# Performance work log

Measured on AMD Instinct MI355X. Metric: run time of the kernel, lower is better.

## Reference

```python
import jax, jax.numpy as jnp
import numpy as np

N, M, D = 1024, 1024, 512


def setup_inputs() -> dict:
    key = jax.random.key(0)
    ks = jax.random.split(key, 12)
    s = 1.0 / np.sqrt(D)
    return {
        "q": jax.random.normal(ks[0], (N, D), jnp.float32),
        "k": jax.random.normal(ks[1], (M, D), jnp.float32),
        "v": jax.random.normal(ks[2], (M, D), jnp.float32),
        "mask": jax.random.randint(ks[3], (N, M), 0, 2) > 0,
        "Wq": jax.random.normal(ks[4], (D, D), jnp.float32) * s,
        "bq": jax.random.normal(ks[5], (D,), jnp.float32) * s,
        "Wk": jax.random.normal(ks[6], (D, D), jnp.float32) * s,
        "bk": jax.random.normal(ks[7], (D,), jnp.float32) * s,
        "Wv": jax.random.normal(ks[8], (D, D), jnp.float32) * s,
        "bv": jax.random.normal(ks[9], (D,), jnp.float32) * s,
        "Ww": jax.random.normal(ks[10], (D,), jnp.float32) * s,
        "bw": jax.random.normal(ks[11], (1,), jnp.float32) * s,
    }


def reference(q, k, v, mask, Wq, bq, Wk, bk, Wv, bv, Ww, bw):
    # Linear projections (torch Linear: x @ W.T + b)
    qp = q @ Wq.T + bq  # [N, D]
    kp = k @ Wk.T + bk  # [M, D]
    vp = v @ Wv.T + bv  # [M, D]
    # Bahdanau additive score: W(tanh(q_n + k_m)) -> [N, M]
    h = jnp.tanh(qp[:, None, :] + kp[None, :, :])  # [N, M, D]
    scores = jnp.einsum('nmd,d->nm', h, Ww) + bw[0]
    scores = jnp.where(mask, scores, jnp.float32(-1000000.0))
    attn = jax.nn.softmax(scores, axis=1)  # softmax over M (dim 1)
    context = jnp.einsum('nm,md->nd', attn, vp)  # [N, D]
    return context
```

## Files before the change

### kernel.cpp

```cpp
#include <hip/hip_runtime.h>
#include <hip/hip_bf16.h>
#include <float.h>


#define NROWS 1024
#define DDIM  512
#define MDIM  1024

typedef __attribute__((ext_vector_type(8))) short s8v;
typedef __attribute__((ext_vector_type(4))) float f4v;
typedef __attribute__((ext_vector_type(2))) float v2f;

__device__ __forceinline__ float bf2f(ushort h) {
    return __uint_as_float(((unsigned)h) << 16);
}
__device__ __forceinline__ ushort2 f2bf2(float a, float b) {
    __hip_bfloat162 t = __float22bfloat162_rn(float2{a, b});
    union { __hip_bfloat162 v; ushort2 u; } c; c.v = t;
    return c.u;
}
__device__ __forceinline__ void hl2(float a, float b, ushort2& h, ushort2& l) {
    h = f2bf2(a, b);
    l = f2bf2(a - bf2f(h.x), b - bf2f(h.y));
}

__global__ __launch_bounds__(256) void proj_gemm(
    const float* __restrict__ q, const float* __restrict__ kk_,
    const float* __restrict__ v,
    const float* __restrict__ Wq, const float* __restrict__ bq,
    const float* __restrict__ Wk, const float* __restrict__ bk,
    const float* __restrict__ Wv, const float* __restrict__ bv,
    float* __restrict__ eq, float* __restrict__ ekT,
    ushort* __restrict__ vph, ushort* __restrict__ vpl,
    float* __restrict__ S, float CS)
{
    __shared__ ushort Ah[4096], Al[4096], Bh[4096], Bl[4096];

    const float* A; const float* B; const float* bias;
    int biasRow;
    if (blockIdx.z == 0)      { A = q;   B = Wq;  bias = bq; biasRow = 0; }
    else if (blockIdx.z == 1) { A = Wk;  B = kk_; bias = bk; biasRow = 1; }
    else                      { A = Wv;  B = v;   bias = bv; biasRow = 1; }

    const int bi = (blockIdx.z == 0) ? blockIdx.x : blockIdx.y;
    const int bj = (blockIdx.z == 0) ? blockIdx.y : blockIdx.x;

    const int t    = threadIdx.x;
    const int lane = t & 63;
    const int w    = t >> 6;
    const int lm   = lane & 15;
    const int lq   = lane >> 4;
    const int i0   = bi * 64;
    const int j0   = bj * 64;
    const int mh   = (w >> 1) * 32;
    const int nh   = (w & 1) * 32;

    if (blockIdx.z == 0) {
        const int jb = blockIdx.x * 8 + blockIdx.y;
        float4 zz = {0.f, 0.f, 0.f, 0.f};
#pragma unroll
        for (int p = 0; p < 8; ++p)
            *(float4*)&S[(size_t)jb * 8192 + (t + p * 256) * 4] = zz;
    }

    f4v acc[2][2] = {{{0.f,0.f,0.f,0.f},{0.f,0.f,0.f,0.f}},
                     {{0.f,0.f,0.f,0.f},{0.f,0.f,0.f,0.f}}};
    float4 pa[4], pb[4];

    const int sr = t >> 4, sc4 = t & 15;
#pragma unroll
    for (int p = 0; p < 4; ++p) {
        int r = sr + p * 16;
        pa[p] = *(const float4*)&A[(size_t)(i0 + r) * DDIM + sc4 * 4];
        pb[p] = *(const float4*)&B[(size_t)(j0 + r) * DDIM + sc4 * 4];
    }

    for (int kc = 0; kc < 8; ++kc) {
        __syncthreads();
#pragma unroll
        for (int p = 0; p < 4; ++p) {
            int r = sr + p * 16;
            int ad = r * 64 + (((sc4 >> 1) ^ (r & 7)) << 3) + (sc4 & 1) * 4;
            ushort2 h01, l01, h23, l23;
            hl2(pa[p].x, pa[p].y, h01, l01);
            hl2(pa[p].z, pa[p].w, h23, l23);
            ushort4 ha = {h01.x, h01.y, h23.x, h23.y};
            ushort4 la = {l01.x, l01.y, l23.x, l23.y};
            *(ushort4*)&Ah[ad] = ha;
            *(ushort4*)&Al[ad] = la;
            hl2(pb[p].x, pb[p].y, h01, l01);
            hl2(pb[p].z, pb[p].w, h23, l23);
            ushort4 hb = {h01.x, h01.y, h23.x, h23.y};
            ushort4 lb = {l01.x, l01.y, l23.x, l23.y};
            *(ushort4*)&Bh[ad] = hb;
            *(ushort4*)&Bl[ad] = lb;
        }
        __syncthreads();
        if (kc < 7) {
            const int k0 = (kc + 1) * 64;
#pragma unroll
            for (int p = 0; p < 4; ++p) {
                int r = sr + p * 16;
                pa[p] = *(const float4*)&A[(size_t)(i0 + r) * DDIM + k0 + sc4 * 4];
                pb[p] = *(const float4*)&B[(size_t)(j0 + r) * DDIM + k0 + sc4 * 4];
            }
        }
#pragma unroll
        for (int ks = 0; ks < 2; ++ks) {
            const int kb = ks * 4 + lq;
            s8v afh[2], afl[2], bfh[2], bfl[2];
#pragma unroll
            for (int g = 0; g < 2; ++g) {
                int ra = mh + g * 16 + lm;
                int rb = nh + g * 16 + lm;
                int aa = ra * 64 + ((kb ^ (ra & 7)) << 3);
                int ab = rb * 64 + ((kb ^ (rb & 7)) << 3);
                afh[g] = *(const s8v*)&Ah[aa];
                afl[g] = *(const s8v*)&Al[aa];
                bfh[g] = *(const s8v*)&Bh[ab];
                bfl[g] = *(const s8v*)&Bl[ab];
            }
#pragma unroll
            for (int mi = 0; mi < 2; ++mi)
#pragma unroll
                for (int ni = 0; ni < 2; ++ni) {
                    acc[mi][ni] = __builtin_amdgcn_mfma_f32_16x16x32_bf16(
                        afh[mi], bfh[ni], acc[mi][ni], 0, 0, 0);
                    acc[mi][ni] = __builtin_amdgcn_mfma_f32_16x16x32_bf16(
                        afh[mi], bfl[ni], acc[mi][ni], 0, 0, 0);
                    acc[mi][ni] = __builtin_amdgcn_mfma_f32_16x16x32_bf16(
                        afl[mi], bfh[ni], acc[mi][ni], 0, 0, 0);
                }
        }
    }

    const float CLAMP = 8192.0f;
#pragma unroll
    for (int mi = 0; mi < 2; ++mi) {
#pragma unroll
        for (int ni = 0; ni < 2; ++ni) {
#pragma unroll
            for (int p = 0; p < 4; ++p) {
                int row = i0 + mh + mi * 16 + lq * 4 + p;
                int col = j0 + nh + ni * 16 + lm;
                float val = acc[mi][ni][p] + (biasRow ? bias[row] : bias[col]);
                if (blockIdx.z == 0) {
                    eq[(size_t)row * 512 + col] =
                        fminf(__builtin_amdgcn_exp2f(val * CS), CLAMP);
                } else if (blockIdx.z == 1) {
                    ekT[(size_t)row * 1024 + col] =
                        fminf(__builtin_amdgcn_exp2f(val * CS), CLAMP);
                } else {
                    ushort2 h2 = f2bf2(val, val);
                    vph[(size_t)row * 1024 + col] = h2.x;
                    ushort2 l2 = f2bf2(val - bf2f(h2.x), 0.f);
                    vpl[(size_t)row * 1024 + col] = l2.x;
                }
            }
        }
    }
}

#define DCH  16
#define SMCH 128
__global__ __launch_bounds__(256) void score_kernel(const float* __restrict__ eq,
                                                    const float* __restrict__ ekT,
                                                    const float* __restrict__ Ww,
                                                    float* __restrict__ S)
{
    __shared__ __align__(16) float ks[DCH * SMCH];
    __shared__ __align__(16) float es[16 * 128];
    __shared__ __align__(16) float wws[128];
    const int t    = threadIdx.x;
    const int lane = t & 63;
    const int w    = t >> 6;
    const int m0   = blockIdx.x * SMCH;
    const int n0   = blockIdx.y * 16;
    const int dbase = blockIdx.z * 128;

    const float SC = 1.220703125e-4f;

#pragma unroll
    for (int p = 0; p < 2; ++p) {
        int idx = t + p * 256;
        int nl = idx >> 5, dd4 = idx & 31;
        float4 e4 = *(const float4*)&eq[(size_t)(n0 + nl) * DDIM + dbase + dd4 * 4];
        float4 e4s = {e4.x * SC, e4.y * SC, e4.z * SC, e4.w * SC};
        *(float4*)&es[nl * 128 + dd4 * 4] = e4s;
    }
    if (t < 128) wws[t] = Ww[dbase + t] * SC;

    const int srow = t >> 5;
    const int scol = (t & 31) * 4;
    const float* gbase = ekT + (size_t)(dbase + srow) * MDIM + m0 + scol;

    float4 ra = *(const float4*)(gbase);
    float4 rb = *(const float4*)(gbase + (size_t)8 * MDIM);
    *(float4*)&ks[srow * SMCH + scol] = ra;
    *(float4*)&ks[(8 + srow) * SMCH + scol] = rb;
    __syncthreads();

    v2f acc[4] = {};
    const v2f cc2 = {1.220703125e-4f, 1.220703125e-4f};

    for (int dc = 0; dc < 128; dc += DCH) {
        if (dc + DCH < 128) {
            const float* g = gbase + (size_t)(dc + DCH) * MDIM;
            ra = *(const float4*)(g);
            rb = *(const float4*)(g + (size_t)8 * MDIM);
        }

#pragma unroll
        for (int dq = 0; dq < DCH; dq += 8) {
            v2f k0 = *(const v2f*)&ks[(dq + 0) * SMCH + lane * 2];
            v2f k1 = *(const v2f*)&ks[(dq + 1) * SMCH + lane * 2];
            v2f k2 = *(const v2f*)&ks[(dq + 2) * SMCH + lane * 2];
            v2f k3 = *(const v2f*)&ks[(dq + 3) * SMCH + lane * 2];
            v2f k4 = *(const v2f*)&ks[(dq + 4) * SMCH + lane * 2];
            v2f k5 = *(const v2f*)&ks[(dq + 5) * SMCH + lane * 2];
            v2f k6 = *(const v2f*)&ks[(dq + 6) * SMCH + lane * 2];
            v2f k7 = *(const v2f*)&ks[(dq + 7) * SMCH + lane * 2];
            float4 wgA = *(const float4*)&wws[dc + dq];
            float4 wgB = *(const float4*)&wws[dc + dq + 4];
#pragma unroll
            for (int nn = 0; nn < 4; ++nn) {
                float4 egA = *(const float4*)&es[(w * 4 + nn) * 128 + dc + dq];
                float4 egB = *(const float4*)&es[(w * 4 + nn) * 128 + dc + dq + 4];
                v2f A0 = __builtin_elementwise_fma(k0, (v2f){egA.x, egA.x}, cc2);
                v2f A1 = __builtin_elementwise_fma(k1, (v2f){egA.y, egA.y}, cc2);
                v2f A2 = __builtin_elementwise_fma(k2, (v2f){egA.z, egA.z}, cc2);
                v2f A3 = __builtin_elementwise_fma(k3, (v2f){egA.w, egA.w}, cc2);
                v2f A4 = __builtin_elementwise_fma(k4, (v2f){egB.x, egB.x}, cc2);
                v2f A5 = __builtin_elementwise_fma(k5, (v2f){egB.y, egB.y}, cc2);
                v2f A6 = __builtin_elementwise_fma(k6, (v2f){egB.z, egB.z}, cc2);
                v2f A7 = __builtin_elementwise_fma(k7, (v2f){egB.w, egB.w}, cc2);
                v2f n01 = __builtin_elementwise_fma((v2f){wgA.y, wgA.y}, A0,
                                                    (v2f){wgA.x, wgA.x} * A1);
                v2f d01 = A0 * A1;
                v2f n23 = __builtin_elementwise_fma((v2f){wgA.w, wgA.w}, A2,
                                                    (v2f){wgA.z, wgA.z} * A3);
                v2f d23 = A2 * A3;
                v2f n45 = __builtin_elementwise_fma((v2f){wgB.y, wgB.y}, A4,
                                                    (v2f){wgB.x, wgB.x} * A5);
                v2f d45 = A4 * A5;
                v2f n67 = __builtin_elementwise_fma((v2f){wgB.w, wgB.w}, A6,
                                                    (v2f){wgB.z, wgB.z} * A7);
                v2f d67 = A6 * A7;
                v2f nA = __builtin_elementwise_fma(n01, d23, n23 * d01);
                v2f dA = d01 * d23;
                v2f nB = __builtin_elementwise_fma(n45, d67, n67 * d45);
                v2f dB = d45 * d67;
                v2f num = __builtin_elementwise_fma(nA, dB, nB * dA);
                v2f den = dA * dB;
                v2f r = {__builtin_amdgcn_rcpf(den.x), __builtin_amdgcn_rcpf(den.y)};
                acc[nn] = __builtin_elementwise_fma(num, r, acc[nn]);
            }
        }

        __syncthreads();
        if (dc + DCH < 128) {
            *(float4*)&ks[srow * SMCH + scol] = ra;
            *(float4*)&ks[(8 + srow) * SMCH + scol] = rb;
        }
        __syncthreads();
    }

    const float C2 = -2.8853900817779268f;
    const int m = m0 + lane * 2;
#pragma unroll
    for (int nn = 0; nn < 4; ++nn) {
        int n = n0 + w * 4 + nn;
        atomicAdd(&S[(size_t)n * MDIM + m],     acc[nn].x * C2);
        atomicAdd(&S[(size_t)n * MDIM + m + 1], acc[nn].y * C2);
    }
}

__global__ __launch_bounds__(256) void combine_kernel(const float* __restrict__ S,
                                                      const int* __restrict__ mask,
                                                      ushort* __restrict__ Ph,
                                                      ushort* __restrict__ Pl,
                                                      float* __restrict__ rsum)
{
    __shared__ float red[4];
    const int n = blockIdx.x, t = threadIdx.x;
    const int lane = t & 63, w = t >> 6;

    float4 s  = *(const float4*)&S[(size_t)n * MDIM + t * 4];
    int4   mk = *(const int4*)&mask[(size_t)n * MDIM + t * 4];
    float p0 = mk.x ? __builtin_amdgcn_exp2f(s.x) : 0.f;
    float p1 = mk.y ? __builtin_amdgcn_exp2f(s.y) : 0.f;
    float p2 = mk.z ? __builtin_amdgcn_exp2f(s.z) : 0.f;
    float p3 = mk.w ? __builtin_amdgcn_exp2f(s.w) : 0.f;

    ushort2 h01, l01, h23, l23;
    hl2(p0, p1, h01, l01);
    hl2(p2, p3, h23, l23);
    ushort4 hv = {h01.x, h01.y, h23.x, h23.y};
    ushort4 lv = {l01.x, l01.y, l23.x, l23.y};
    *(ushort4*)&Ph[(size_t)n * MDIM + t * 4] = hv;
    *(ushort4*)&Pl[(size_t)n * MDIM + t * 4] = lv;

    float rs = (p0 + p1) + (p2 + p3);
#pragma unroll
    for (int off = 32; off; off >>= 1) rs += __shfl_xor(rs, off);
    if (lane == 0) red[w] = rs;
    __syncthreads();
    if (t == 0) rsum[n] = (red[0] + red[1]) + (red[2] + red[3]);
}

__global__ __launch_bounds__(256) void ctx_gemm(const ushort* __restrict__ Ph,
                                                const ushort* __restrict__ Pl,
                                                const ushort* __restrict__ vph,
                                                const ushort* __restrict__ vpl,
                                                const float* __restrict__ rsum,
                                                float* __restrict__ out)
{
    __shared__ __align__(16) float red[3 * 64 * 4];
    const int t    = threadIdx.x;
    const int lane = t & 63;
    const int w    = t >> 6;
    const int lm   = lane & 15;
    const int lq   = lane >> 4;
    const int d0   = blockIdx.x * 16;
    const int n0   = blockIdx.y * 16;
    const int mb   = w * 256;

    const ushort* pAh = Ph  + (size_t)(n0 + lm) * MDIM + mb + lq * 8;
    const ushort* pAl = Pl  + (size_t)(n0 + lm) * MDIM + mb + lq * 8;
    const ushort* pBh = vph + (size_t)(d0 + lm) * MDIM + mb + lq * 8;
    const ushort* pBl = vpl + (size_t)(d0 + lm) * MDIM + mb + lq * 8;

    f4v acc = {0.f, 0.f, 0.f, 0.f};
#pragma unroll 4
    for (int m0 = 0; m0 < 256; m0 += 32) {
        s8v ah = *(const s8v*)(pAh + m0);
        s8v al = *(const s8v*)(pAl + m0);
        s8v bh = *(const s8v*)(pBh + m0);
        s8v bl = *(const s8v*)(pBl + m0);
        acc = __builtin_amdgcn_mfma_f32_16x16x32_bf16(ah, bh, acc, 0, 0, 0);
        acc = __builtin_amdgcn_mfma_f32_16x16x32_bf16(ah, bl, acc, 0, 0, 0);
        acc = __builtin_amdgcn_mfma_f32_16x16x32_bf16(al, bh, acc, 0, 0, 0);
    }

    if (w > 0) *(f4v*)&red[((w - 1) * 64 + lane) * 4] = acc;
    __syncthreads();
    if (w == 0) {
#pragma unroll
        for (int i = 0; i < 3; ++i)
            acc += *(const f4v*)&red[(i * 64 + lane) * 4];
#pragma unroll
        for (int p = 0; p < 4; ++p) {
            int nrow = n0 + lq * 4 + p;
            float inv = __builtin_amdgcn_rcpf(rsum[nrow]);
            out[(size_t)nrow * DDIM + d0 + lm] = acc[p] * inv;
        }
    }
}

extern "C" void kernel_launch(void* const* d_in, const int* in_sizes, int n_in,
                              void* d_out, int out_size, void* d_ws, size_t ws_size,
                              hipStream_t stream)
{
    const float* q    = (const float*)d_in[0];
    const float* k    = (const float*)d_in[1];
    const float* v    = (const float*)d_in[2];
    const int*   mask = (const int*)d_in[3];
    const float* Wq   = (const float*)d_in[4];
    const float* bq   = (const float*)d_in[5];
    const float* Wk   = (const float*)d_in[6];
    const float* bk   = (const float*)d_in[7];
    const float* Wv   = (const float*)d_in[8];
    const float* bv   = (const float*)d_in[9];
    const float* Ww   = (const float*)d_in[10];

    float* ws    = (float*)d_ws;
    float* eq    = ws;
    float* ekT   = ws + 524288;
    ushort* vph  = (ushort*)(ws + 1048576);
    ushort* vpl  = (ushort*)(ws + 1310720);
    float* S     = ws + 1572864;
    float* rsum  = ws + 2621440;
    ushort* Ph   = (ushort*)ws;
    ushort* Pl   = (ushort*)(ws + 524288);
    float* out   = (float*)d_out;

    const float CS = 2.8853900817779268f;

    proj_gemm<<<dim3(16, 8, 3), dim3(256), 0, stream>>>(q, k, v, Wq, bq, Wk, bk,
                                                        Wv, bv, eq, ekT,
                                                        vph, vpl, S, CS);
    score_kernel<<<dim3(8, 64, 4), dim3(256), 0, stream>>>(eq, ekT, Ww, S);
    combine_kernel<<<dim3(1024), dim3(256), 0, stream>>>(S, mask, Ph, Pl, rsum);
    ctx_gemm<<<dim3(32, 64), dim3(256), 0, stream>>>(Ph, Pl, vph, vpl, rsum, out);
}
```

Before: 178.0 us.

## Widen score tile to 4 columns per lane with direct global-to-LDS loads

Each lane of the score kernel now computes 4 key columns instead of 2, doubling the m-tile to 256 and halving the grid in x. Reuse of the q-side and weight values held in registers per LDS read goes up. Key tiles are now staged with global_load_lds instead of register prefetch, so the software double-buffering that overlapped the next chunk's load with compute is gone. The q-side scale factor is folded into the projection epilogue. This trades fewer blocks and no load/compute overlap for more arithmetic per LDS access, plus higher register pressure.

After: 203.2 us. +14.2%, slower.

```diff
diff --git a/kernel.cpp b/kernel.cpp
--- a/kernel.cpp
+++ b/kernel.cpp
@@ -22,6 +22,12 @@
 __device__ __forceinline__ void hl2(float a, float b, ushort2& h, ushort2& l) {
     h = f2bf2(a, b);
     l = f2bf2(a - bf2f(h.x), b - bf2f(h.y));
+}
+
+__device__ __forceinline__ void load_lds16(const float* g, float* l) {
+    __builtin_amdgcn_global_load_lds(
+        (const __attribute__((address_space(1))) void*)g,
+        (__attribute__((address_space(3))) void*)l, 16, 0, 0);
 }
 
 __global__ __launch_bounds__(256) void proj_gemm(
@@ -135,6 +141,7 @@
     }
 
     const float CLAMP = 8192.0f;
+    const float SCw   = 1.220703125e-4f;
 #pragma unroll
     for (int mi = 0; mi < 2; ++mi) {
 #pragma unroll
@@ -146,7 +153,7 @@
                 float val = acc[mi][ni][p] + (biasRow ? bias[row] : bias[col]);
                 if (blockIdx.z == 0) {
                     eq[(size_t)row * 512 + col] =
-                        fminf(__builtin_amdgcn_exp2f(val * CS), CLAMP);
+                        fminf(__builtin_amdgcn_exp2f(val * CS), CLAMP) * SCw;
                 } else if (blockIdx.z == 1) {
                     ekT[(size_t)row * 1024 + col] =
                         fminf(__builtin_amdgcn_exp2f(val * CS), CLAMP);
@@ -162,7 +169,7 @@
 }
 
 #define DCH  16
-#define SMCH 128
+#define SMCH 256
 __global__ __launch_bounds__(256) void score_kernel(const float* __restrict__ eq,
                                                     const float* __restrict__ ekT,
                                                     const float* __restrict__ Ww,
@@ -184,94 +191,98 @@
     for (int p = 0; p < 2; ++p) {
         int idx = t + p * 256;
         int nl = idx >> 5, dd4 = idx & 31;
-        float4 e4 = *(const float4*)&eq[(size_t)(n0 + nl) * DDIM + dbase + dd4 * 4];
-        float4 e4s = {e4.x * SC, e4.y * SC, e4.z * SC, e4.w * SC};
-        *(float4*)&es[nl * 128 + dd4 * 4] = e4s;
+        *(float4*)&es[nl * 128 + dd4 * 4] =
+            *(const float4*)&eq[(size_t)(n0 + nl) * DDIM + dbase + dd4 * 4];
     }
     if (t < 128) wws[t] = Ww[dbase + t] * SC;
 
-    const int srow = t >> 5;
-    const int scol = (t & 31) * 4;
-    const float* gbase = ekT + (size_t)(dbase + srow) * MDIM + m0 + scol;
-
-    float4 ra = *(const float4*)(gbase);
-    float4 rb = *(const float4*)(gbase + (size_t)8 * MDIM);
-    *(float4*)&ks[srow * SMCH + scol] = ra;
-    *(float4*)&ks[(8 + srow) * SMCH + scol] = rb;
-    __syncthreads();
-
-    v2f acc[4] = {};
-    const v2f cc2 = {1.220703125e-4f, 1.220703125e-4f};
+    f4v acc[4] = {};
+    const f4v cc4 = {1.220703125e-4f, 1.220703125e-4f,
+                     1.220703125e-4f, 1.220703125e-4f};
 
     for (int dc = 0; dc < 128; dc += DCH) {
-        if (dc + DCH < 128) {
-            const float* g = gbase + (size_t)(dc + DCH) * MDIM;
-            ra = *(const float4*)(g);
-            rb = *(const float4*)(g + (size_t)8 * MDIM);
-        }
+        __syncthreads();
+#pragma unroll
+        for (int i = 0; i < 4; ++i) {
+            int row = w * 4 + i;
+            const float* g = ekT + (size_t)(dbase + dc + row) * MDIM
+                             + m0 + lane * 4;
+            load_lds16(g, &ks[row * SMCH]);
+        }
+        __syncthreads();
 
 #pragma unroll
         for (int dq = 0; dq < DCH; dq += 8) {
-            v2f k0 = *(const v2f*)&ks[(dq + 0) * SMCH + lane * 2];
-            v2f k1 = *(const v2f*)&ks[(dq + 1) * SMCH + lane * 2];
-            v2f k2 = *(const v2f*)&ks[(dq + 2) * SMCH + lane * 2];
-            v2f k3 = *(const v2f*)&ks[(dq + 3) * SMCH + lane * 2];
-            v2f k4 = *(const v2f*)&ks[(dq + 4) * SMCH + lane * 2];
-            v2f k5 = *(const v2f*)&ks[(dq + 5) * SMCH + lane * 2];
-            v2f k6 = *(const v2f*)&ks[(dq + 6) * SMCH + lane * 2];
-            v2f k7 = *(const v2f*)&ks[(dq + 7) * SMCH + lane * 2];
+            f4v k0 = *(const f4v*)&ks[(dq + 0) * SMCH + lane * 4];
+            f4v k1 = *(const f4v*)&ks[(dq + 1) * SMCH + lane * 4];
+            f4v k2 = *(const f4v*)&ks[(dq + 2) * SMCH + lane * 4];
+            f4v k3 = *(const f4v*)&ks[(dq + 3) * SMCH + lane * 4];
+            f4v k4 = *(const f4v*)&ks[(dq + 4) * SMCH + lane * 4];
+            f4v k5 = *(const f4v*)&ks[(dq + 5) * SMCH + lane * 4];
+            f4v k6 = *(const f4v*)&ks[(dq + 6) * SMCH + lane * 4];
+            f4v k7 = *(const f4v*)&ks[(dq + 7) * SMCH + lane * 4];
             float4 wgA = *(const float4*)&wws[dc + dq];
             float4 wgB = *(const float4*)&wws[dc + dq + 4];
 #pragma unroll
             for (int nn = 0; nn < 4; ++nn) {
                 float4 egA = *(const float4*)&es[(w * 4 + nn) * 128 + dc + dq];
                 float4 egB = *(const float4*)&es[(w * 4 + nn) * 128 + dc + dq + 4];
-                v2f A0 = __builtin_elementwise_fma(k0, (v2f){egA.x, egA.x}, cc2);
-                v2f A1 = __builtin_elementwise_fma(k1, (v2f){egA.y, egA.y}, cc2);
-                v2f A2 = __builtin_elementwise_fma(k2, (v2f){egA.z, egA.z}, cc2);
-                v2f A3 = __builtin_elementwise_fma(k3, (v2f){egA.w, egA.w}, cc2);
-                v2f A4 = __builtin_elementwise_fma(k4, (v2f){egB.x, egB.x}, cc2);
-                v2f A5 = __builtin_elementwise_fma(k5, (v2f){egB.y, egB.y}, cc2);
-                v2f A6 = __builtin_elementwise_fma(k6, (v2f){egB.z, egB.z}, cc2);
-                v2f A7 = __builtin_elementwise_fma(k7, (v2f){egB.w, egB.w}, cc2);
-                v2f n01 = __builtin_elementwise_fma((v2f){wgA.y, wgA.y}, A0,
-                                                    (v2f){wgA.x, wgA.x} * A1);
-                v2f d01 = A0 * A1;
-                v2f n23 = __builtin_elementwise_fma((v2f){wgA.w, wgA.w}, A2,
-                                                    (v2f){wgA.z, wgA.z} * A3);
-                v2f d23 = A2 * A3;
-                v2f n45 = __builtin_elementwise_fma((v2f){wgB.y, wgB.y}, A4,
-                                                    (v2f){wgB.x, wgB.x} * A5);
-                v2f d45 = A4 * A5;
-                v2f n67 = __builtin_elementwise_fma((v2f){wgB.w, wgB.w}, A6,
-                                                    (v2f){wgB.z, wgB.z} * A7);
-                v2f d67 = A6 * A7;
-                v2f nA = __builtin_elementwise_fma(n01, d23, n23 * d01);
-                v2f dA = d01 * d23;
-                v2f nB = __builtin_elementwise_fma(n45, d67, n67 * d45);
-                v2f dB = d45 * d67;
-                v2f num = __builtin_elementwise_fma(nA, dB, nB * dA);
-                v2f den = dA * dB;
-                v2f r = {__builtin_amdgcn_rcpf(den.x), __builtin_amdgcn_rcpf(den.y)};
+                f4v A0 = __builtin_elementwise_fma(k0,
+                         (f4v){egA.x, egA.x, egA.x, egA.x}, cc4);
+                f4v A1 = __builtin_elementwise_fma(k1,
+                         (f4v){egA.y, egA.y, egA.y, egA.y}, cc4);
+                f4v A2 = __builtin_elementwise_fma(k2,
+                         (f4v){egA.z, egA.z, egA.z, egA.z}, cc4);
+                f4v A3 = __builtin_elementwise_fma(k3,
+                         (f4v){egA.w, egA.w, egA.w, egA.w}, cc4);
+                f4v A4 = __builtin_elementwise_fma(k4,
+                         (f4v){egB.x, egB.x, egB.x, egB.x}, cc4);
+                f4v A5 = __builtin_elementwise_fma(k5,
+                         (f4v){egB.y, egB.y, egB.y, egB.y}, cc4);
+                f4v A6 = __builtin_elementwise_fma(k6,
+                         (f4v){egB.z, egB.z, egB.z, egB.z}, cc4);
+                f4v A7 = __builtin_elementwise_fma(k7,
+                         (f4v){egB.w, egB.w, egB.w, egB.w}, cc4);
+                f4v n01 = __builtin_elementwise_fma(
+                    (f4v){wgA.y, wgA.y, wgA.y, wgA.y}, A0,
+                    (f4v){wgA.x, wgA.x, wgA.x, wgA.x} * A1);
+                f4v d01 = A0 * A1;
+                f4v n23 = __builtin_elementwise_fma(
+                    (f4v){wgA.w, wgA.w, wgA.w, wgA.w}, A2,
+                    (f4v){wgA.z, wgA.z, wgA.z, wgA.z} * A3);
+                f4v d23 = A2 * A3;
+                f4v n45 = __builtin_elementwise_fma(
+                    (f4v){wgB.y, wgB.y, wgB.y, wgB.y}, A4,
+                    (f4v){wgB.x, wgB.x, wgB.x, wgB.x} * A5);
+                f4v d45 = A4 * A5;
+                f4v n67 = __builtin_elementwise_fma(
+                    (f4v){wgB.w, wgB.w, wgB.w, wgB.w}, A6,
+                    (f4v){wgB.z, wgB.z, wgB.z, wgB.z} * A7);
+                f4v d67 = A6 * A7;
+                f4v nA = __builtin_elementwise_fma(n01, d23, n23 * d01);
+                f4v dA = d01 * d23;
+                f4v nB = __builtin_elementwise_fma(n45, d67, n67 * d45);
+                f4v dB = d45 * d67;
+                f4v num = __builtin_elementwise_fma(nA, dB, nB * dA);
+                f4v den = dA * dB;
+                f4v r = {__builtin_amdgcn_rcpf(den.x),
+                         __builtin_amdgcn_rcpf(den.y),
+                         __builtin_amdgcn_rcpf(den.z),
+                         __builtin_amdgcn_rcpf(den.w)};
                 acc[nn] = __builtin_elementwise_fma(num, r, acc[nn]);
             }
         }
-
-        __syncthreads();
-        if (dc + DCH < 128) {
-            *(float4*)&ks[srow * SMCH + scol] = ra;
-            *(float4*)&ks[(8 + srow) * SMCH + scol] = rb;
-        }
-        __syncthreads();
     }
 
     const float C2 = -2.8853900817779268f;
-    const int m = m0 + lane * 2;
+    const int m = m0 + lane * 4;
 #pragma unroll
     for (int nn = 0; nn < 4; ++nn) {
         int n = n0 + w * 4 + nn;
         atomicAdd(&S[(size_t)n * MDIM + m],     acc[nn].x * C2);
         atomicAdd(&S[(size_t)n * MDIM + m + 1], acc[nn].y * C2);
+        atomicAdd(&S[(size_t)n * MDIM + m + 2], acc[nn].z * C2);
+        atomicAdd(&S[(size_t)n * MDIM + m + 3], acc[nn].w * C2);
     }
 }
 
@@ -389,7 +400,7 @@
     proj_gemm<<<dim3(16, 8, 3), dim3(256), 0, stream>>>(q, k, v, Wq, bq, Wk, bk,
                                                         Wv, bv, eq, ekT,
                                                         vph, vpl, S, CS);
-    score_kernel<<<dim3(8, 64, 4), dim3(256), 0, stream>>>(eq, ekT, Ww, S);
+    score_kernel<<<dim3(4, 64, 4), dim3(256), 0, stream>>>(eq, ekT, Ww, S);
     combine_kernel<<<dim3(1024), dim3(256), 0, stream>>>(S, mask, Ph, Pl, rsum);
     ctx_gemm<<<dim3(32, 64), dim3(256), 0, stream>>>(Ph, Pl, vph, vpl, rsum, out);
 }
```

## Load key exponentials directly into registers in score kernel, dropping LDS staging

Applied to the files above, without the earlier changes.

The score kernel stops staging ekT tiles through shared memory with double syncthreads per chunk. Each lane now reads its own two key columns straight from global memory into registers, software-pipelined across two 8-row halves. The SC scaling of eq moves into the projection kernel's epilogue so the score kernel copies eq unchanged. The trade-off is that each of the four waves re-reads the same ekT values from global/L2 instead of sharing one LDS copy, and register pressure goes up.

Measured after the change: 179.9 us. No clear change (+1.1%).

```diff
diff --git a/kernel.cpp b/kernel.cpp
--- a/kernel.cpp
+++ b/kernel.cpp
@@ -135,6 +135,7 @@
     }
 
     const float CLAMP = 8192.0f;
+    const float SCw   = 1.220703125e-4f;
 #pragma unroll
     for (int mi = 0; mi < 2; ++mi) {
 #pragma unroll
@@ -146,7 +147,7 @@
                 float val = acc[mi][ni][p] + (biasRow ? bias[row] : bias[col]);
                 if (blockIdx.z == 0) {
                     eq[(size_t)row * 512 + col] =
-                        fminf(__builtin_amdgcn_exp2f(val * CS), CLAMP);
+                        fminf(__builtin_amdgcn_exp2f(val * CS), CLAMP) * SCw;
                 } else if (blockIdx.z == 1) {
                     ekT[(size_t)row * 1024 + col] =
                         fminf(__builtin_amdgcn_exp2f(val * CS), CLAMP);
@@ -161,14 +162,53 @@
     }
 }
 
-#define DCH  16
 #define SMCH 128
+
+#define TREE8(K0,K1,K2,K3,K4,K5,K6,K7,DCQ)                                     \
+    {                                                                          \
+        float4 wgA = *(const float4*)&wws[(DCQ)];                              \
+        float4 wgB = *(const float4*)&wws[(DCQ) + 4];                          \
+        _Pragma("unroll")                                                      \
+        for (int nn = 0; nn < 4; ++nn) {                                       \
+            float4 egA = *(const float4*)&es[(wrow + nn) * 128 + (DCQ)];       \
+            float4 egB = *(const float4*)&es[(wrow + nn) * 128 + (DCQ) + 4];   \
+            v2f A0 = __builtin_elementwise_fma(K0, (v2f){egA.x, egA.x}, cc2);  \
+            v2f A1 = __builtin_elementwise_fma(K1, (v2f){egA.y, egA.y}, cc2);  \
+            v2f A2 = __builtin_elementwise_fma(K2, (v2f){egA.z, egA.z}, cc2);  \
+            v2f A3 = __builtin_elementwise_fma(K3, (v2f){egA.w, egA.w}, cc2);  \
+            v2f A4 = __builtin_elementwise_fma(K4, (v2f){egB.x, egB.x}, cc2);  \
+            v2f A5 = __builtin_elementwise_fma(K5, (v2f){egB.y, egB.y}, cc2);  \
+            v2f A6 = __builtin_elementwise_fma(K6, (v2f){egB.z, egB.z}, cc2);  \
+            v2f A7 = __builtin_elementwise_fma(K7, (v2f){egB.w, egB.w}, cc2);  \
+            v2f n01 = __builtin_elementwise_fma((v2f){wgA.y, wgA.y}, A0,       \
+                                                (v2f){wgA.x, wgA.x} * A1);     \
+            v2f d01 = A0 * A1;                                                 \
+            v2f n23 = __builtin_elementwise_fma((v2f){wgA.w, wgA.w}, A2,       \
+                                                (v2f){wgA.z, wgA.z} * A3);     \
+            v2f d23 = A2 * A3;                                                 \
+            v2f n45 = __builtin_elementwise_fma((v2f){wgB.y, wgB.y}, A4,       \
+                                                (v2f){wgB.x, wgB.x} * A5);     \
+            v2f d45 = A4 * A5;                                                 \
+            v2f n67 = __builtin_elementwise_fma((v2f){wgB.w, wgB.w}, A6,       \
+                                                (v2f){wgB.z, wgB.z} * A7);     \
+            v2f d67 = A6 * A7;                                                 \
+            v2f nA = __builtin_elementwise_fma(n01, d23, n23 * d01);           \
+            v2f dA = d01 * d23;                                                \
+            v2f nB = __builtin_elementwise_fma(n45, d67, n67 * d45);           \
+            v2f dB = d45 * d67;                                                \
+            v2f num = __builtin_elementwise_fma(nA, dB, nB * dA);              \
+            v2f den = dA * dB;                                                 \
+            v2f r = {__builtin_amdgcn_rcpf(den.x),                             \
+                     __builtin_amdgcn_rcpf(den.y)};                            \
+            acc[nn] = __builtin_elementwise_fma(num, r, acc[nn]);              \
+        }                                                                      \
+    }
+
 __global__ __launch_bounds__(256) void score_kernel(const float* __restrict__ eq,
                                                     const float* __restrict__ ekT,
                                                     const float* __restrict__ Ww,
                                                     float* __restrict__ S)
 {
-    __shared__ __align__(16) float ks[DCH * SMCH];
     __shared__ __align__(16) float es[16 * 128];
     __shared__ __align__(16) float wws[128];
     const int t    = threadIdx.x;
@@ -177,6 +217,7 @@
     const int m0   = blockIdx.x * SMCH;
     const int n0   = blockIdx.y * 16;
     const int dbase = blockIdx.z * 128;
+    const int wrow = w * 4;
 
     const float SC = 1.220703125e-4f;
 
@@ -184,92 +225,60 @@
     for (int p = 0; p < 2; ++p) {
         int idx = t + p * 256;
         int nl = idx >> 5, dd4 = idx & 31;
-        float4 e4 = *(const float4*)&eq[(size_t)(n0 + nl) * DDIM + dbase + dd4 * 4];
-        float4 e4s = {e4.x * SC, e4.y * SC, e4.z * SC, e4.w * SC};
-        *(float4*)&es[nl * 128 + dd4 * 4] = e4s;
+        *(float4*)&es[nl * 128 + dd4 * 4] =
+            *(const float4*)&eq[(size_t)(n0 + nl) * DDIM + dbase + dd4 * 4];
     }
     if (t < 128) wws[t] = Ww[dbase + t] * SC;
 
-    const int srow = t >> 5;
-    const int scol = (t & 31) * 4;
-    const float* gbase = ekT + (size_t)(dbase + srow) * MDIM + m0 + scol;
-
-    float4 ra = *(const float4*)(gbase);
-    float4 rb = *(const float4*)(gbase + (size_t)8 * MDIM);
-    *(float4*)&ks[srow * SMCH + scol] = ra;
-    *(float4*)&ks[(8 + srow) * SMCH + scol] = rb;
+    const float* gk = ekT + (size_t)dbase * MDIM + m0 + lane * 2;
+
+    v2f a0 = *(const v2f*)(gk + (size_t)0 * MDIM);
+    v2f a1 = *(const v2f*)(gk + (size_t)1 * MDIM);
+    v2f a2 = *(const v2f*)(gk + (size_t)2 * MDIM);
+    v2f a3 = *(const v2f*)(gk + (size_t)3 * MDIM);
+    v2f a4 = *(const v2f*)(gk + (size_t)4 * MDIM);
+    v2f a5 = *(const v2f*)(gk + (size_t)5 * MDIM);
+    v2f a6 = *(const v2f*)(gk + (size_t)6 * MDIM);
+    v2f a7 = *(const v2f*)(gk + (size_t)7 * MDIM);
+
     __syncthreads();
 
     v2f acc[4] = {};
     const v2f cc2 = {1.220703125e-4f, 1.220703125e-4f};
 
-    for (int dc = 0; dc < 128; dc += DCH) {
-        if (dc + DCH < 128) {
-            const float* g = gbase + (size_t)(dc + DCH) * MDIM;
-            ra = *(const float4*)(g);
-            rb = *(const float4*)(g + (size_t)8 * MDIM);
-        }
-
-#pragma unroll
-        for (int dq = 0; dq < DCH; dq += 8) {
-            v2f k0 = *(const v2f*)&ks[(dq + 0) * SMCH + lane * 2];
-            v2f k1 = *(const v2f*)&ks[(dq + 1) * SMCH + lane * 2];
-            v2f k2 = *(const v2f*)&ks[(dq + 2) * SMCH + lane * 2];
-            v2f k3 = *(const v2f*)&ks[(dq + 3) * SMCH + lane * 2];
-            v2f k4 = *(const v2f*)&ks[(dq + 4) * SMCH + lane * 2];
-            v2f k5 = *(const v2f*)&ks[(dq + 5) * SMCH + lane * 2];
-            v2f k6 = *(const v2f*)&ks[(dq + 6) * SMCH + lane * 2];
-            v2f k7 = *(const v2f*)&ks[(dq + 7) * SMCH + lane * 2];
-            float4 wgA = *(const float4*)&wws[dc + dq];
-            float4 wgB = *(const float4*)&wws[dc + dq + 4];
-#pragma unroll
-            for (int nn = 0; nn < 4; ++nn) {
-                float4 egA = *(const float4*)&es[(w * 4 + nn) * 128 + dc + dq];
-                float4 egB = *(const float4*)&es[(w * 4 + nn) * 128 + dc + dq + 4];
-                v2f A0 = __builtin_elementwise_fma(k0, (v2f){egA.x, egA.x}, cc2);
-                v2f A1 = __builtin_elementwise_fma(k1, (v2f){egA.y, egA.y}, cc2);
-                v2f A2 = __builtin_elementwise_fma(k2, (v2f){egA.z, egA.z}, cc2);
-                v2f A3 = __builtin_elementwise_fma(k3, (v2f){egA.w, egA.w}, cc2);
-                v2f A4 = __builtin_elementwise_fma(k4, (v2f){egB.x, egB.x}, cc2);
-                v2f A5 = __builtin_elementwise_fma(k5, (v2f){egB.y, egB.y}, cc2);
-                v2f A6 = __builtin_elementwise_fma(k6, (v2f){egB.z, egB.z}, cc2);
-                v2f A7 = __builtin_elementwise_fma(k7, (v2f){egB.w, egB.w}, cc2);
-                v2f n01 = __builtin_elementwise_fma((v2f){wgA.y, wgA.y}, A0,
-                                                    (v2f){wgA.x, wgA.x} * A1);
-                v2f d01 = A0 * A1;
-                v2f n23 = __builtin_elementwise_fma((v2f){wgA.w, wgA.w}, A2,
-                                                    (v2f){wgA.z, wgA.z} * A3);
-                v2f d23 = A2 * A3;
-                v2f n45 = __builtin_elementwise_fma((v2f){wgB.y, wgB.y}, A4,
-                                                    (v2f){wgB.x, wgB.x} * A5);
-                v2f d45 = A4 * A5;
-                v2f n67 = __builtin_elementwise_fma((v2f){wgB.w, wgB.w}, A6,
-                                                    (v2f){wgB.z, wgB.z} * A7);
-                v2f d67 = A6 * A7;
-                v2f nA = __builtin_elementwise_fma(n01, d23, n23 * d01);
-                v2f dA = d01 * d23;
-                v2f nB = __builtin_elementwise_fma(n45, d67, n67 * d45);
-                v2f dB = d45 * d67;
-                v2f num = __builtin_elementwise_fma(nA, dB, nB * dA);
-                v2f den = dA * dB;
-                v2f r = {__builtin_amdgcn_rcpf(den.x), __builtin_amdgcn_rcpf(den.y)};
-                acc[nn] = __builtin_elementwise_fma(num, r, acc[nn]);
-            }
-        }
-
-        __syncthreads();
-        if (dc + DCH < 128) {
-            *(float4*)&ks[srow * SMCH + scol] = ra;
-            *(float4*)&ks[(8 + srow) * SMCH + scol] = rb;
-        }
-        __syncthreads();
+    for (int dc = 0; dc < 128; dc += 16) {
+        const float* g8 = gk + (size_t)(dc + 8) * MDIM;
+        v2f b0 = *(const v2f*)(g8 + (size_t)0 * MDIM);
+        v2f b1 = *(const v2f*)(g8 + (size_t)1 * MDIM);
+        v2f b2 = *(const v2f*)(g8 + (size_t)2 * MDIM);
+        v2f b3 = *(const v2f*)(g8 + (size_t)3 * MDIM);
+        v2f b4 = *(const v2f*)(g8 + (size_t)4 * MDIM);
+        v2f b5 = *(const v2f*)(g8 + (size_t)5 * MDIM);
+        v2f b6 = *(const v2f*)(g8 + (size_t)6 * MDIM);
+        v2f b7 = *(const v2f*)(g8 + (size_t)7 * MDIM);
+
+        TREE8(a0, a1, a2, a3, a4, a5, a6, a7, dc)
+
+        if (dc + 16 < 128) {
+            const float* g16 = gk + (size_t)(dc + 16) * MDIM;
+            a0 = *(const v2f*)(g16 + (size_t)0 * MDIM);
+            a1 = *(const v2f*)(g16 + (size_t)1 * MDIM);
+            a2 = *(const v2f*)(g16 + (size_t)2 * MDIM);
+            a3 = *(const v2f*)(g16 + (size_t)3 * MDIM);
+            a4 = *(const v2f*)(g16 + (size_t)4 * MDIM);
+            a5 = *(const v2f*)(g16 + (size_t)5 * MDIM);
+            a6 = *(const v2f*)(g16 + (size_t)6 * MDIM);
+            a7 = *(const v2f*)(g16 + (size_t)7 * MDIM);
+        }
+
+        TREE8(b0, b1, b2, b3, b4, b5, b6, b7, dc + 8)
     }
 
     const float C2 = -2.8853900817779268f;
     const int m = m0 + lane * 2;
 #pragma unroll
     for (int nn = 0; nn < 4; ++nn) {
-        int n = n0 + w * 4 + nn;
+        int n = n0 + wrow + nn;
         atomicAdd(&S[(size_t)n * MDIM + m],     acc[nn].x * C2);
         atomicAdd(&S[(size_t)n * MDIM + m + 1], acc[nn].y * C2);
     }
```
